# Kernel optimization log

Measured on AMD Instinct MI355X. Metric: run time of the kernel, lower is better.

## Reference

```python
import jax, jax.numpy as jnp
import numpy as np
import math

B, S, H, NH = 8, 2048, 256, 4
DH = H // NH
EPS = 1e-12


def setup_inputs() -> dict:
    key = jax.random.key(0)
    ks = jax.random.split(key, 20)
    g = lambda k, shape: (jax.random.normal(k, shape, jnp.float32) * 0.02)
    inp = {
        "hidden": jax.random.normal(ks[0], (B, S, H), jnp.float32),
        "Wq": g(ks[1], (H, H)), "bq": jnp.zeros((H,), jnp.float32),
        "Wk": g(ks[2], (H, H)), "bk": jnp.zeros((H,), jnp.float32),
        "Wv": g(ks[3], (H, H)), "bv": jnp.zeros((H,), jnp.float32),
        "Wo": g(ks[4], (H, H)), "bo": jnp.zeros((H,), jnp.float32),
        "W1": g(ks[5], (4 * H, H)), "b1": jnp.zeros((4 * H,), jnp.float32),
        "W2": g(ks[6], (H, 4 * H)), "b2": jnp.zeros((H,), jnp.float32),
        "ln1_w": jnp.ones((H,), jnp.float32), "ln1_b": jnp.zeros((H,), jnp.float32),
        "ln2_w": jnp.ones((H,), jnp.float32), "ln2_b": jnp.zeros((H,), jnp.float32),
        "mask": jax.random.randint(ks[7], (B, S), 0, 2, jnp.int32),
    }
    return inp


def _layernorm(x, w, b):
    u = x.mean(-1, keepdims=True)
    s = ((x - u) ** 2).mean(-1, keepdims=True)
    return w * (x - u) / jnp.sqrt(s + EPS) + b


def _gelu_tanh(h):
    return 0.5 * h * (1.0 + jnp.tanh(math.sqrt(2.0 / math.pi) * (h + 0.044715 * h ** 3)))


def _block(hidden, mask, Wq, bq, Wk, bk, Wv, bv, Wo, bo, W1, b1, W2, b2,
           ln1_w, ln1_b, ln2_w, ln2_b):
    # --- attention sublayer (pre-norm + residual) ---
    x = _layernorm(hidden, ln1_w, ln1_b)
    def heads(W, b):  # [B,S,H] -> [B,NH,S,DH]
        return (x @ W.T + b).reshape(B, S, NH, DH).transpose(0, 2, 1, 3)
    q, k, v = heads(Wq, bq), heads(Wk, bk), heads(Wv, bv)
    corr = jnp.einsum("bhqd,bhkd->bhqk", q, k) / math.sqrt(DH)
    # torch code masks QUERY rows: mask [B,S] broadcast over heads and keys
    corr = jnp.where(mask[:, None, :, None] == 0, -1e9, corr)
    prob = jax.nn.softmax(corr, axis=-1)
    attn = jnp.einsum("bhqk,bhkd->bhqd", prob, v)
    attn = attn.transpose(0, 2, 1, 3).reshape(B, S, H) @ Wo.T + bo
    hidden = hidden + attn
    # --- FFN sublayer (pre-norm + residual) ---
    y = _layernorm(hidden, ln2_w, ln2_b)
    h1 = y @ W1.T + b1
    ff = _gelu_tanh(h1) @ W2.T + b2
    return hidden + ff


def reference(hidden, Wq, bq, Wk, bk, Wv, bv, Wo, bo, W1, b1, W2, b2,
              ln1_w, ln1_b, ln2_w, ln2_b, mask):
    return _block(hidden, mask, Wq, bq, Wk, bk, Wv, bv, Wo, bo,
                  W1, b1, W2, b2, ln1_w, ln1_b, ln2_w, ln2_b)
```

## Files before the change

kernel.cpp:

```cpp
#include <hip/hip_runtime.h>
#include <hip/hip_bf16.h>
#include <cstdint>
#include <cstddef>

constexpr int CB  = 8;
constexpr int CS  = 2048;
constexpr int CH  = 256;
constexpr int CNH = 4;
constexpr int CDH = 64;
constexpr int CT  = CB * CS;

typedef __attribute__((ext_vector_type(8)))  __bf16 bf16x8;
typedef __attribute__((ext_vector_type(4)))  float  f32x4;
typedef __attribute__((ext_vector_type(16))) float  f32x16;
typedef __attribute__((ext_vector_type(2)))  int    i32x2;

__device__ __forceinline__ float b2f(unsigned short u) {
    union { float f; unsigned int i; } v; v.i = ((unsigned int)u) << 16; return v.f;
}
__device__ __forceinline__ unsigned short f2b(float f) {
    union { float f; unsigned int i; } v; v.f = f;
    unsigned int r = v.i + 0x7FFFu + ((v.i >> 16) & 1u);
    return (unsigned short)(r >> 16);
}
__device__ __forceinline__ unsigned short f2b_fast(float f) {
    union { float f; unsigned int i; } v; v.f = f;
    return (unsigned short)((v.i + 0x8000u) >> 16);
}
__device__ __forceinline__ unsigned int packbf(float a, float b) {
    return (unsigned int)f2b_fast(a) | ((unsigned int)f2b_fast(b) << 16);
}
__device__ __forceinline__ float fexp2(float x) {
#if __has_builtin(__builtin_amdgcn_exp2f)
    return __builtin_amdgcn_exp2f(x);
#else
    float r; asm("v_exp_f32 %0, %1" : "=v"(r) : "v"(x)); return r;
#endif
}
__device__ __forceinline__ f32x4 mfma16(bf16x8 a, bf16x8 b, f32x4 c) {
    return __builtin_amdgcn_mfma_f32_16x16x32_bf16(a, b, c, 0, 0, 0);
}
__device__ __forceinline__ f32x16 mfma32(bf16x8 a, bf16x8 b, f32x16 c) {
    return __builtin_amdgcn_mfma_f32_32x32x16_bf16(a, b, c, 0, 0, 0);
}
__device__ __forceinline__ f32x16 zero16() {
    f32x16 z;
    #pragma unroll
    for (int i = 0; i < 16; ++i) z[i] = 0.f;
    return z;
}

#define GLOAD_LDS16(gptr, lptr)                                                        \
    __builtin_amdgcn_global_load_lds((const __attribute__((address_space(1))) void*)(gptr), \
                                     (__attribute__((address_space(3))) void*)(lptr), 16, 0, 0)

#define QSCALE 0.1803368801111204f

__global__ __launch_bounds__(256) void detect_kernel(
    const unsigned short* __restrict__ h, int* __restrict__ flag)
{
    __shared__ int s_bad;
    const int tid = threadIdx.x;
    if (tid == 0) s_bad = 0;
    __syncthreads();
    bool bad = false;
    for (int i = tid; i < 2048; i += 256) {
        float v = b2f(h[i]);
        if (!(fabsf(v) < 1e25f)) bad = true;
    }
    if (bad) s_bad = 1;
    __syncthreads();
    if (tid == 0) *flag = s_bad;
}

struct CvtArgs6  { const void* src[6];  void* dst[6];  int n[6]; };
struct CvtArgs11 { const void* src[11]; void* dst[11]; int n[11]; };

__global__ __launch_bounds__(256) void cvt_to_bf16_k(const int* __restrict__ flag, CvtArgs6 a)
{
    const int seg = blockIdx.y, n = a.n[seg];
    const bool inf32 = (*flag != 0);
    const float* sf = (const float*)a.src[seg];
    const unsigned short* sb = (const unsigned short*)a.src[seg];
    unsigned short* d = (unsigned short*)a.dst[seg];
    for (int i = (blockIdx.x * 256 + threadIdx.x) * 4; i < n; i += gridDim.x * 1024) {
        ushort4 o;
        if (inf32) {
            float4 v = *(const float4*)(sf + i);
            o.x = f2b(v.x); o.y = f2b(v.y); o.z = f2b(v.z); o.w = f2b(v.w);
        } else {
            o = *(const ushort4*)(sb + i);
        }
        *(ushort4*)(d + i) = o;
    }
}

__global__ __launch_bounds__(256) void cvt_to_f32_k(const int* __restrict__ flag, CvtArgs11 a)
{
    const int seg = blockIdx.y, n = a.n[seg];
    const bool inf32 = (*flag != 0);
    const float* sf = (const float*)a.src[seg];
    const unsigned short* sb = (const unsigned short*)a.src[seg];
    float* d = (float*)a.dst[seg];
    for (int i = (blockIdx.x * 256 + threadIdx.x) * 4; i < n; i += gridDim.x * 1024) {
        float4 o;
        if (inf32) {
            o = *(const float4*)(sf + i);
        } else {
            ushort4 v = *(const ushort4*)(sb + i);
            o.x = b2f(v.x); o.y = b2f(v.y); o.z = b2f(v.z); o.w = b2f(v.w);
        }
        *(float4*)(d + i) = o;
    }
}

__global__ __launch_bounds__(256) void ln_kernel(
    const float* __restrict__ x, const float* __restrict__ w,
    const float* __restrict__ b, unsigned short* __restrict__ out)
{
    const int wave = threadIdx.x >> 6, lane = threadIdx.x & 63;
    const int token = blockIdx.x * 4 + wave;
    const int c = lane * 4;
    const size_t rowo = (size_t)token * CH + c;
    float4 u = *(const float4*)(x + rowo);
    float v0 = u.x, v1 = u.y, v2 = u.z, v3 = u.w;
    float s = v0 + v1 + v2 + v3;
    float q = v0*v0 + v1*v1 + v2*v2 + v3*v3;
    #pragma unroll
    for (int m = 1; m < 64; m <<= 1) { s += __shfl_xor(s, m, 64); q += __shfl_xor(q, m, 64); }
    float mean = s * (1.0f/256.0f);
    float var  = q * (1.0f/256.0f) - mean*mean;
    float inv  = rsqrtf(var + 1e-12f);
    float4 ww = *(const float4*)(w + c);
    float4 bb = *(const float4*)(b + c);
    ushort4 o;
    o.x = f2b(ww.x * (v0-mean)*inv + bb.x);
    o.y = f2b(ww.y * (v1-mean)*inv + bb.y);
    o.z = f2b(ww.z * (v2-mean)*inv + bb.z);
    o.w = f2b(ww.w * (v3-mean)*inv + bb.w);
    *(ushort4*)(out + rowo) = o;
}

template<bool GELU, bool RESID, bool HEADSTORE, bool OUTF32, bool OUTDYN>
__device__ __forceinline__ void gemm_core(
    const unsigned short* __restrict__ A, const unsigned short* __restrict__ W,
    const float* __restrict__ bias, const float* __restrict__ resid,
    void* __restrict__ out, const int* __restrict__ flag,
    int K, int N, int m0, int n0, float oscale)
{
    __shared__ __align__(16) unsigned short lA[128*32];
    __shared__ __align__(16) unsigned short lB[128*32];
    const int tid  = threadIdx.x;
    const int lane = tid & 63;
    const int wave = tid >> 6;
    const int wr = (wave >> 1) * 64;
    const int wc = (wave & 1) * 64;
    const int g = lane >> 4, r16 = lane & 15;
    const int lrow = lane >> 2;
    const int lch  = lane & 3;

    const f32x4 zero = {0.f, 0.f, 0.f, 0.f};
    f32x4 acc[4][4];
    #pragma unroll
    for (int m = 0; m < 4; ++m)
        #pragma unroll
        for (int n = 0; n < 4; ++n) acc[m][n] = zero;

    for (int k0 = 0; k0 < K; k0 += 32) {
        #pragma unroll
        for (int i = 0; i < 2; ++i) {
            int chunk = wave + i * 4;
            int row = chunk * 16 + lrow;
            const unsigned short* ga = A + (size_t)(m0 + row) * K + k0 + lch * 8;
            GLOAD_LDS16(ga, &lA[chunk * 512]);
            const unsigned short* gw = W + (size_t)(n0 + row) * K + k0 + lch * 8;
            GLOAD_LDS16(gw, &lB[chunk * 512]);
        }
        __syncthreads();
        bf16x8 af[4], wf[4];
        #pragma unroll
        for (int m = 0; m < 4; ++m) af[m] = *(const bf16x8*)&lA[(wr + m*16 + r16) * 32 + g * 8];
        #pragma unroll
        for (int n = 0; n < 4; ++n) wf[n] = *(const bf16x8*)&lB[(wc + n*16 + r16) * 32 + g * 8];
        #pragma unroll
        for (int m = 0; m < 4; ++m)
            #pragma unroll
            for (int n = 0; n < 4; ++n)
                acc[m][n] = mfma16(af[m], wf[n], acc[m][n]);
        __syncthreads();
    }

    const bool of32dyn = OUTDYN ? (*flag != 0) : false;
    #pragma unroll
    for (int n = 0; n < 4; ++n) {
        int col = n0 + wc + n*16 + r16;
        float bv = bias[col];
        #pragma unroll
        for (int m = 0; m < 4; ++m) {
            int row0 = m0 + wr + m*16 + g*4;
            #pragma unroll
            for (int r = 0; r < 4; ++r) {
                int row = row0 + r;
                float v = (acc[m][n][r] + bv) * oscale;
                if (GELU) {
                    float a = 0.79788456080286541f * (v + 0.044715f * v * v * v);
                    v = v * (1.0f / (1.0f + __expf(-2.0f * a)));
                }
                if (RESID) v += resid[(size_t)row * N + col];
                size_t oidx;
                if (HEADSTORE) {
                    int hh = col >> 6, d = col & 63;
                    int bb = row >> 11, ss = row & 2047;
                    oidx = ((((size_t)bb * CNH + hh) * CS) + ss) * CDH + d;
                } else {
                    oidx = (size_t)row * N + col;
                }
                if (OUTF32)      ((float*)out)[oidx] = v;
                else if (OUTDYN) {
                    if (of32dyn) ((float*)out)[oidx] = v;
                    else         ((unsigned short*)out)[oidx] = f2b(v);
                }
                else             ((unsigned short*)out)[oidx] = f2b(v);
            }
        }
    }
}

__global__ __launch_bounds__(256) void k_qkv(
    const unsigned short* __restrict__ xhat,
    const unsigned short* Wq, const float* bq, unsigned short* q,
    const unsigned short* Wk, const float* bk, unsigned short* k,
    const unsigned short* Wv, const float* bv, unsigned short* v)
{
    const unsigned short* W  = blockIdx.z == 0 ? Wq : (blockIdx.z == 1 ? Wk : Wv);
    const float*          bi = blockIdx.z == 0 ? bq : (blockIdx.z == 1 ? bk : bv);
    unsigned short*       o  = blockIdx.z == 0 ? q  : (blockIdx.z == 1 ? k  : v);
    const float osc = blockIdx.z == 0 ? QSCALE : 1.0f;
    gemm_core<false, false, true, false, false>(xhat, W, bi, nullptr, o, nullptr,
                                                CH, CH, blockIdx.x * 128, blockIdx.y * 128, osc);
}

__global__ __launch_bounds__(256) void k_oproj(
    const unsigned short* __restrict__ A, const unsigned short* __restrict__ W,
    const float* __restrict__ bias, const float* __restrict__ resid,
    float* __restrict__ out)
{
    gemm_core<false, true, false, true, false>(A, W, bias, resid, out, nullptr,
                                               CH, CH, blockIdx.x * 128, blockIdx.y * 128, 1.0f);
}

__global__ __launch_bounds__(256) void k_ffn1(
    const unsigned short* __restrict__ A, const unsigned short* __restrict__ W,
    const float* __restrict__ bias, unsigned short* __restrict__ out)
{
    gemm_core<true, false, false, false, false>(A, W, bias, nullptr, out, nullptr,
                                                CH, 4*CH, blockIdx.x * 128, blockIdx.y * 128, 1.0f);
}

__global__ __launch_bounds__(256) void k_ffn2(
    const unsigned short* __restrict__ A, const unsigned short* __restrict__ W,
    const float* __restrict__ bias, const float* __restrict__ resid,
    void* __restrict__ out, const int* __restrict__ flag)
{
    gemm_core<false, true, false, false, true>(A, W, bias, resid, out, flag,
                                               4*CH, CH, blockIdx.x * 128, blockIdx.y * 128, 1.0f);
}

__global__ __launch_bounds__(256) void vtrans_kernel(
    const unsigned short* __restrict__ v, unsigned short* __restrict__ vt)
{
    __shared__ unsigned short T[64 * 72];
    const int bh = blockIdx.y, s0 = blockIdx.x * 64, tid = threadIdx.x;
    const size_t ibase = (size_t)bh * CS * CDH;
    const size_t obase = (size_t)bh * CDH * CS;
    #pragma unroll
    for (int i = 0; i < 2; ++i) {
        int t2 = tid + i * 256;
        int row = t2 >> 3, ch = t2 & 7;
        uint4 dv = *(const uint4*)(v + ibase + (size_t)(s0 + row) * CDH + ch * 8);
        *(uint4*)&T[row * 72 + ch * 8] = dv;
    }
    __syncthreads();
    #pragma unroll
    for (int i = 0; i < 2; ++i) {
        int t2 = tid + i * 256;
        int d = t2 >> 3, ch = t2 & 7;
        unsigned short tmp[8];
        #pragma unroll
        for (int j = 0; j < 8; ++j) tmp[j] = T[(ch * 8 + j) * 72 + d];
        *(uint4*)(vt + obase + (size_t)d * CS + s0 + ch * 8) = *(uint4*)tmp;
    }
}

__global__ __launch_bounds__(512, 4) void attn_kernel(
    const unsigned short* __restrict__ Q, const unsigned short* __restrict__ Kp,
    const unsigned short* __restrict__ Vt, const int* __restrict__ mask,
    unsigned short* __restrict__ out)
{
    __shared__ __align__(16) char lds[65536];

    const int tid = threadIdx.x, lane = tid & 63, wave = tid >> 6;
    const int qb = wave >> 1, kh = wave & 1;
    const int r32 = lane & 31, hi = lane >> 5;
    const int bh = blockIdx.y, bb = bh >> 2, hh = bh & 3;
    const int q0 = blockIdx.x * 128;
    const size_t baseQ = (size_t)bh * CS * CDH;
    const size_t baseT = (size_t)bh * CDH * CS;

    const int qrow = q0 + qb * 32 + r32;
    bf16x8 qf[4];
    {
        const bool live = (mask[bb * CS + qrow] != 0);
        #pragma unroll
        for (int dw = 0; dw < 4; ++dw) {
            uint4 v = {0u, 0u, 0u, 0u};
            if (live) v = *(const uint4*)(Q + baseQ + (size_t)qrow * CDH + dw * 16 + hi * 8);
            qf[dw] = *(bf16x8*)&v;
        }
    }

#define STAGE(BUF, KT) do {                                                             \
        _Pragma("unroll")                                                               \
        for (int i = 0; i < 2; ++i) {                                                   \
            const int slot0 = i * 512 + wave * 64;                                      \
            const int slot  = slot0 + lane;                                             \
            const int kw = slot >> 7, kk2 = slot & 127;                                 \
            GLOAD_LDS16(Kp + baseQ + (size_t)((KT) + kk2) * CDH + kw * 8,               \
                        lds + (BUF) * 16384 + slot0 * 16);                              \
            const int vc = slot >> 6, vd = slot & 63;                                   \
            GLOAD_LDS16(Vt + baseT + (size_t)vd * CS + (KT) + vc * 8,                   \
                        lds + 32768 + (BUF) * 16384 + slot0 * 16);                      \
        } } while (0)

    f32x16 o0 = zero16(), o1 = zero16();
    float psum = 0.f;

    STAGE(0, 0);
    __syncthreads();

    for (int t = 0; t < CS / 128; ++t) {
        const int buf = t & 1;
        const int kt = t * 128;
        if (t + 1 < CS / 128) STAGE(buf ^ 1, kt + 128);

        const char* kbase = lds + buf * 16384;
        const char* vbase = lds + 32768 + buf * 16384;

        f32x16 sT0 = zero16(), sT1 = zero16();
        __builtin_amdgcn_s_setprio(1);
        #pragma unroll
        for (int dw = 0; dw < 4; ++dw) {
            const char* cb = kbase + (dw * 2 + hi) * 2048;
            bf16x8 k0 = *(const bf16x8*)(cb + (kh * 64 + r32) * 16);
            bf16x8 k1 = *(const bf16x8*)(cb + (kh * 64 + 32 + r32) * 16);
            sT0 = mfma32(k0, qf[dw], sT0);
            sT1 = mfma32(k1, qf[dw], sT1);
        }
        __builtin_amdgcn_s_setprio(0);

#define PROCKB(SREG, KB) do {                                                           \
            float p[16];                                                                \
            _Pragma("unroll")                                                           \
            for (int r = 0; r < 16; ++r) { p[r] = fexp2((SREG)[r]); psum += p[r]; }     \
            _Pragma("unroll")                                                           \
            for (int w = 0; w < 2; ++w) {                                               \
                unsigned int a01 = packbf(p[w*8+0], p[w*8+1]);                          \
                unsigned int a23 = packbf(p[w*8+2], p[w*8+3]);                          \
                unsigned int b01 = packbf(p[w*8+4], p[w*8+5]);                          \
                unsigned int b23 = packbf(p[w*8+6], p[w*8+7]);                          \
                unsigned int ap0, ap1, ap2, ap3;                                        \
                {                                                                       \
                    i32x2 s1 = __builtin_amdgcn_permlane32_swap((int)a01, (int)b01, false, false); \
                    i32x2 s2 = __builtin_amdgcn_permlane32_swap((int)a23, (int)b23, false, false); \
                    ap0 = (unsigned int)s1.x; ap2 = (unsigned int)s1.y;                 \
                    ap1 = (unsigned int)s2.x; ap3 = (unsigned int)s2.y;                 \
                }                                                                       \
                union { unsigned int u[4]; bf16x8 v; } apv;                             \
                apv.u[0] = ap0; apv.u[1] = ap1; apv.u[2] = ap2; apv.u[3] = ap3;         \
                const char* vb2 = vbase + ((kh * 4 + (KB) * 2 + w) * 2 + hi) * 1024;    \
                bf16x8 v0 = *(const bf16x8*)(vb2 + r32 * 16);                           \
                bf16x8 v1 = *(const bf16x8*)(vb2 + (32 + r32) * 16);                    \
                o0 = mfma32(apv.v, v0, o0);                                             \
                o1 = mfma32(apv.v, v1, o1);                                             \
            } } while (0)

        PROCKB(sT0, 0);
        PROCKB(sT1, 1);
#undef PROCKB

        __syncthreads();
    }

    float ps = psum + __shfl_xor(psum, 32, 64);
    float* lsum = (float*)(lds + 32768);
    float* Oex  = (float*)lds;
    if (lane < 32) lsum[(qb * 2 + kh) * 32 + r32] = ps;
    if (kh == 1) {
        #pragma unroll
        for (int r = 0; r < 16; ++r) {
            const int qr = (r & 3) + 8 * (r >> 2) + 4 * hi;
            Oex[(qb * 32 + qr) * 64 + r32]      = o0[r];
            Oex[(qb * 32 + qr) * 64 + 32 + r32] = o1[r];
        }
    }
    __syncthreads();
    if (kh == 0) {
        #pragma unroll
        for (int r = 0; r < 16; ++r) {
            const int qr = (r & 3) + 8 * (r >> 2) + 4 * hi;
            const float l = lsum[(qb * 2 + 0) * 32 + qr] + lsum[(qb * 2 + 1) * 32 + qr];
            const float inv = 1.0f / l;
            const float u0 = (o0[r] + Oex[(qb * 32 + qr) * 64 + r32]) * inv;
            const float u1 = (o1[r] + Oex[(qb * 32 + qr) * 64 + 32 + r32]) * inv;
            const size_t ob = (size_t)(bb * CS + q0 + qb * 32 + qr) * CH + hh * CDH;
            out[ob + r32]      = f2b(u0);
            out[ob + 32 + r32] = f2b(u1);
        }
    }
#undef STAGE
}

extern "C" void kernel_launch(void* const* d_in, const int* in_sizes, int n_in,
                              void* d_out, int out_size, void* d_ws, size_t ws_size,
                              hipStream_t stream)
{
    const void* hidden = d_in[0];
    const void* Wq = d_in[1];  const void* bq = d_in[2];
    const void* Wk = d_in[3];  const void* bk = d_in[4];
    const void* Wv = d_in[5];  const void* bv = d_in[6];
    const void* Wo = d_in[7];  const void* bo = d_in[8];
    const void* W1 = d_in[9];  const void* b1 = d_in[10];
    const void* W2 = d_in[11]; const void* b2 = d_in[12];
    const void* ln1w = d_in[13]; const void* ln1b = d_in[14];
    const void* ln2w = d_in[15]; const void* ln2b = d_in[16];
    const int* mask = (const int*)d_in[17];

    char* ws = (char*)d_ws;
    const size_t KB = 1u << 10, MB = 1u << 20;
    int*            flag  = (int*)ws;
    float*          bqf   = (float*)(ws + 4*KB);
    float*          bkf   = (float*)(ws + 8*KB);
    float*          bvf   = (float*)(ws + 12*KB);
    float*          bof   = (float*)(ws + 16*KB);
    float*          b1f   = (float*)(ws + 20*KB);
    float*          b2f_  = (float*)(ws + 28*KB);
    float*          ln1wf = (float*)(ws + 32*KB);
    float*          ln1bf = (float*)(ws + 36*KB);
    float*          ln2wf = (float*)(ws + 40*KB);
    float*          ln2bf = (float*)(ws + 44*KB);
    unsigned short* Wqb   = (unsigned short*)(ws + 1*MB);
    unsigned short* Wkb   = (unsigned short*)(ws + 1*MB + 256*KB);
    unsigned short* Wvb   = (unsigned short*)(ws + 1*MB + 512*KB);
    unsigned short* Wob   = (unsigned short*)(ws + 1*MB + 768*KB);
    unsigned short* W1b   = (unsigned short*)(ws + 2*MB);
    unsigned short* W2b   = (unsigned short*)(ws + 2*MB + 512*KB);
    float*          hf32  = (float*)(ws + 3*MB);
    unsigned short* xhat  = (unsigned short*)(ws + 19*MB);
    unsigned short* qb    = (unsigned short*)(ws + 27*MB);
    unsigned short* kb    = (unsigned short*)(ws + 35*MB);
    unsigned short* vb    = (unsigned short*)(ws + 43*MB);
    unsigned short* attnb = xhat;
    float*          hid2f = (float*)(ws + 35*MB);
    unsigned short* vtb   = (unsigned short*)(ws + 51*MB);
    unsigned short* yhat  = qb;
    unsigned short* h1g   = (unsigned short*)(ws + 51*MB);

    dim3 blk(256);
    detect_kernel<<<1, blk, 0, stream>>>((const unsigned short*)hidden, flag);

    CvtArgs6 cw;
    cw.src[0]=Wq;  cw.dst[0]=Wqb; cw.n[0]=CH*CH;
    cw.src[1]=Wk;  cw.dst[1]=Wkb; cw.n[1]=CH*CH;
    cw.src[2]=Wv;  cw.dst[2]=Wvb; cw.n[2]=CH*CH;
    cw.src[3]=Wo;  cw.dst[3]=Wob; cw.n[3]=CH*CH;
    cw.src[4]=W1;  cw.dst[4]=W1b; cw.n[4]=4*CH*CH;
    cw.src[5]=W2;  cw.dst[5]=W2b; cw.n[5]=4*CH*CH;
    cvt_to_bf16_k<<<dim3(64, 6), blk, 0, stream>>>(flag, cw);

    CvtArgs11 cf;
    cf.src[0]=hidden; cf.dst[0]=hf32;  cf.n[0]=CT*CH;
    cf.src[1]=bq;     cf.dst[1]=bqf;   cf.n[1]=CH;
    cf.src[2]=bk;     cf.dst[2]=bkf;   cf.n[2]=CH;
    cf.src[3]=bv;     cf.dst[3]=bvf;   cf.n[3]=CH;
    cf.src[4]=bo;     cf.dst[4]=bof;   cf.n[4]=CH;
    cf.src[5]=b1;     cf.dst[5]=b1f;   cf.n[5]=4*CH;
    cf.src[6]=b2;     cf.dst[6]=b2f_;  cf.n[6]=CH;
    cf.src[7]=ln1w;   cf.dst[7]=ln1wf; cf.n[7]=CH;
    cf.src[8]=ln1b;   cf.dst[8]=ln1bf; cf.n[8]=CH;
    cf.src[9]=ln2w;   cf.dst[9]=ln2wf; cf.n[9]=CH;
    cf.src[10]=ln2b;  cf.dst[10]=ln2bf;cf.n[10]=CH;
    cvt_to_f32_k<<<dim3(512, 11), blk, 0, stream>>>(flag, cf);

    ln_kernel<<<CT / 4, blk, 0, stream>>>(hf32, ln1wf, ln1bf, xhat);
    k_qkv<<<dim3(CT / 128, CH / 128, 3), blk, 0, stream>>>(xhat, Wqb, bqf, qb,
                                                           Wkb, bkf, kb, Wvb, bvf, vb);
    vtrans_kernel<<<dim3(CS / 64, CB * CNH), blk, 0, stream>>>(vb, vtb);
    attn_kernel<<<dim3(CS / 128, CB * CNH), dim3(512), 0, stream>>>(qb, kb, vtb, mask, attnb);
    k_oproj<<<dim3(CT / 128, CH / 128), blk, 0, stream>>>(attnb, Wob, bof, hf32, hid2f);
    ln_kernel<<<CT / 4, blk, 0, stream>>>(hid2f, ln2wf, ln2bf, yhat);
    k_ffn1<<<dim3(CT / 128, (4 * CH) / 128), blk, 0, stream>>>(yhat, W1b, b1f, h1g);
    k_ffn2<<<dim3(CT / 128, CH / 128), blk, 0, stream>>>(h1g, W2b, b2f_, hid2f,
                                                         d_out, flag);
}
```

Baseline: 167.8 us.

## Store residual stream in bf16 and reorder GEMM grids for weight reuse

```diff
diff --git a/kernel.cpp b/kernel.cpp
--- a/kernel.cpp
+++ b/kernel.cpp
@@ -23,12 +23,10 @@
     unsigned int r = v.i + 0x7FFFu + ((v.i >> 16) & 1u);
     return (unsigned short)(r >> 16);
 }
-__device__ __forceinline__ unsigned short f2b_fast(float f) {
-    union { float f; unsigned int i; } v; v.f = f;
-    return (unsigned short)((v.i + 0x8000u) >> 16);
-}
 __device__ __forceinline__ unsigned int packbf(float a, float b) {
-    return (unsigned int)f2b_fast(a) | ((unsigned int)f2b_fast(b) << 16);
+    float2 t; t.x = a; t.y = b;
+    __hip_bfloat162 h = __float22bfloat162_rn(t);
+    union { __hip_bfloat162 h; unsigned int u; } c; c.h = h; return c.u;
 }
 __device__ __forceinline__ float fexp2(float x) {
 #if __has_builtin(__builtin_amdgcn_exp2f)
@@ -73,10 +71,10 @@
     if (tid == 0) *flag = s_bad;
 }
 
-struct CvtArgs6  { const void* src[6];  void* dst[6];  int n[6]; };
-struct CvtArgs11 { const void* src[11]; void* dst[11]; int n[11]; };
-
-__global__ __launch_bounds__(256) void cvt_to_bf16_k(const int* __restrict__ flag, CvtArgs6 a)
+struct CvtW { const void* src[7]; void* dst[7]; int n[7]; };
+struct CvtB { const void* src[10]; void* dst[10]; int n[10]; };
+
+__global__ __launch_bounds__(256) void cvt_wb_k(const int* __restrict__ flag, CvtW a)
 {
     const int seg = blockIdx.y, n = a.n[seg];
     const bool inf32 = (*flag != 0);
@@ -95,14 +93,15 @@
     }
 }
 
-__global__ __launch_bounds__(256) void cvt_to_f32_k(const int* __restrict__ flag, CvtArgs11 a)
+__global__ __launch_bounds__(256) void cvt_bf_k(const int* __restrict__ flag, CvtB a)
 {
     const int seg = blockIdx.y, n = a.n[seg];
     const bool inf32 = (*flag != 0);
     const float* sf = (const float*)a.src[seg];
     const unsigned short* sb = (const unsigned short*)a.src[seg];
     float* d = (float*)a.dst[seg];
-    for (int i = (blockIdx.x * 256 + threadIdx.x) * 4; i < n; i += gridDim.x * 1024) {
+    const int i = threadIdx.x * 4;
+    if (i < n) {
         float4 o;
         if (inf32) {
             o = *(const float4*)(sf + i);
@@ -115,15 +114,15 @@
 }
 
 __global__ __launch_bounds__(256) void ln_kernel(
-    const float* __restrict__ x, const float* __restrict__ w,
+    const unsigned short* __restrict__ x, const float* __restrict__ w,
     const float* __restrict__ b, unsigned short* __restrict__ out)
 {
     const int wave = threadIdx.x >> 6, lane = threadIdx.x & 63;
     const int token = blockIdx.x * 4 + wave;
     const int c = lane * 4;
     const size_t rowo = (size_t)token * CH + c;
-    float4 u = *(const float4*)(x + rowo);
-    float v0 = u.x, v1 = u.y, v2 = u.z, v3 = u.w;
+    ushort4 u = *(const ushort4*)(x + rowo);
+    float v0 = b2f(u.x), v1 = b2f(u.y), v2 = b2f(u.z), v3 = b2f(u.w);
     float s = v0 + v1 + v2 + v3;
     float q = v0*v0 + v1*v1 + v2*v2 + v3*v3;
     #pragma unroll
@@ -141,10 +140,10 @@
     *(ushort4*)(out + rowo) = o;
 }
 
-template<bool GELU, bool RESID, bool HEADSTORE, bool OUTF32, bool OUTDYN>
+template<bool GELU, bool RESID, bool HEADSTORE, bool OUTDYN>
 __device__ __forceinline__ void gemm_core(
     const unsigned short* __restrict__ A, const unsigned short* __restrict__ W,
-    const float* __restrict__ bias, const float* __restrict__ resid,
+    const float* __restrict__ bias, const unsigned short* __restrict__ resid,
     void* __restrict__ out, const int* __restrict__ flag,
     int K, int N, int m0, int n0, float oscale)
 {
@@ -206,7 +205,7 @@
                     float a = 0.79788456080286541f * (v + 0.044715f * v * v * v);
                     v = v * (1.0f / (1.0f + __expf(-2.0f * a)));
                 }
-                if (RESID) v += resid[(size_t)row * N + col];
+                if (RESID) v += b2f(resid[(size_t)row * N + col]);
                 size_t oidx;
                 if (HEADSTORE) {
                     int hh = col >> 6, d = col & 63;
@@ -215,12 +214,8 @@
                 } else {
                     oidx = (size_t)row * N + col;
                 }
-                if (OUTF32)      ((float*)out)[oidx] = v;
-                else if (OUTDYN) {
-                    if (of32dyn) ((float*)out)[oidx] = v;
-                    else         ((unsigned short*)out)[oidx] = f2b(v);
-                }
-                else             ((unsigned short*)out)[oidx] = f2b(v);
+                if (OUTDYN && of32dyn) ((float*)out)[oidx] = v;
+                else                   ((unsigned short*)out)[oidx] = f2b(v);
             }
         }
     }
@@ -232,38 +227,41 @@
     const unsigned short* Wk, const float* bk, unsigned short* k,
     const unsigned short* Wv, const float* bv, unsigned short* v)
 {
-    const unsigned short* W  = blockIdx.z == 0 ? Wq : (blockIdx.z == 1 ? Wk : Wv);
-    const float*          bi = blockIdx.z == 0 ? bq : (blockIdx.z == 1 ? bk : bv);
-    unsigned short*       o  = blockIdx.z == 0 ? q  : (blockIdx.z == 1 ? k  : v);
-    const float osc = blockIdx.z == 0 ? QSCALE : 1.0f;
-    gemm_core<false, false, true, false, false>(xhat, W, bi, nullptr, o, nullptr,
-                                                CH, CH, blockIdx.x * 128, blockIdx.y * 128, osc);
+    const int z  = blockIdx.x % 3;
+    const int n0 = (blockIdx.x / 3) * 128;
+    const int m0 = blockIdx.y * 128;
+    const unsigned short* W  = z == 0 ? Wq : (z == 1 ? Wk : Wv);
+    const float*          bi = z == 0 ? bq : (z == 1 ? bk : bv);
+    unsigned short*       o  = z == 0 ? q  : (z == 1 ? k  : v);
+    const float osc = z == 0 ? QSCALE : 1.0f;
+    gemm_core<false, false, true, false>(xhat, W, bi, nullptr, o, nullptr,
+                                         CH, CH, m0, n0, osc);
 }
 
 __global__ __launch_bounds__(256) void k_oproj(
     const unsigned short* __restrict__ A, const unsigned short* __restrict__ W,
-    const float* __restrict__ bias, const float* __restrict__ resid,
-    float* __restrict__ out)
-{
-    gemm_core<false, true, false, true, false>(A, W, bias, resid, out, nullptr,
-                                               CH, CH, blockIdx.x * 128, blockIdx.y * 128, 1.0f);
+    const float* __restrict__ bias, const unsigned short* __restrict__ resid,
+    unsigned short* __restrict__ out)
+{
+    gemm_core<false, true, false, false>(A, W, bias, resid, out, nullptr,
+                                         CH, CH, blockIdx.y * 128, blockIdx.x * 128, 1.0f);
 }
 
 __global__ __launch_bounds__(256) void k_ffn1(
     const unsigned short* __restrict__ A, const unsigned short* __restrict__ W,
     const float* __restrict__ bias, unsigned short* __restrict__ out)
 {
-    gemm_core<true, false, false, false, false>(A, W, bias, nullptr, out, nullptr,
-                                                CH, 4*CH, blockIdx.x * 128, blockIdx.y * 128, 1.0f);
+    gemm_core<true, false, false, false>(A, W, bias, nullptr, out, nullptr,
+                                         CH, 4*CH, blockIdx.y * 128, blockIdx.x * 128, 1.0f);
 }
 
 __global__ __launch_bounds__(256) void k_ffn2(
     const unsigned short* __restrict__ A, const unsigned short* __restrict__ W,
-    const float* __restrict__ bias, const float* __restrict__ resid,
+    const float* __restrict__ bias, const unsigned short* __restrict__ resid,
     void* __restrict__ out, const int* __restrict__ flag)
 {
-    gemm_core<false, true, false, false, true>(A, W, bias, resid, out, flag,
-                                               4*CH, CH, blockIdx.x * 128, blockIdx.y * 128, 1.0f);
+    gemm_core<false, true, false, true>(A, W, bias, resid, out, flag,
+                                        4*CH, CH, blockIdx.y * 128, blockIdx.x * 128, 1.0f);
 }
 
 __global__ __launch_bounds__(256) void vtrans_kernel(
@@ -454,51 +452,51 @@
     unsigned short* Wob   = (unsigned short*)(ws + 1*MB + 768*KB);
     unsigned short* W1b   = (unsigned short*)(ws + 2*MB);
     unsigned short* W2b   = (unsigned short*)(ws + 2*MB + 512*KB);
-    float*          hf32  = (float*)(ws + 3*MB);
-    unsigned short* xhat  = (unsigned short*)(ws + 19*MB);
-    unsigned short* qb    = (unsigned short*)(ws + 27*MB);
-    unsigned short* kb    = (unsigned short*)(ws + 35*MB);
-    unsigned short* vb    = (unsigned short*)(ws + 43*MB);
+    unsigned short* hb16  = (unsigned short*)(ws + 3*MB);
+    unsigned short* xhat  = (unsigned short*)(ws + 11*MB);
+    unsigned short* qb    = (unsigned short*)(ws + 19*MB);
+    unsigned short* kb    = (unsigned short*)(ws + 27*MB);
+    unsigned short* vb    = (unsigned short*)(ws + 35*MB);
+    unsigned short* vtb   = (unsigned short*)(ws + 43*MB);
     unsigned short* attnb = xhat;
-    float*          hid2f = (float*)(ws + 35*MB);
-    unsigned short* vtb   = (unsigned short*)(ws + 51*MB);
-    unsigned short* yhat  = qb;
+    unsigned short* hid2b = qb;
+    unsigned short* yhat  = kb;
     unsigned short* h1g   = (unsigned short*)(ws + 51*MB);
 
     dim3 blk(256);
     detect_kernel<<<1, blk, 0, stream>>>((const unsigned short*)hidden, flag);
 
-    CvtArgs6 cw;
-    cw.src[0]=Wq;  cw.dst[0]=Wqb; cw.n[0]=CH*CH;
-    cw.src[1]=Wk;  cw.dst[1]=Wkb; cw.n[1]=CH*CH;
-    cw.src[2]=Wv;  cw.dst[2]=Wvb; cw.n[2]=CH*CH;
-    cw.src[3]=Wo;  cw.dst[3]=Wob; cw.n[3]=CH*CH;
-    cw.src[4]=W1;  cw.dst[4]=W1b; cw.n[4]=4*CH*CH;
-    cw.src[5]=W2;  cw.dst[5]=W2b; cw.n[5]=4*CH*CH;
-    cvt_to_bf16_k<<<dim3(64, 6), blk, 0, stream>>>(flag, cw);
-
-    CvtArgs11 cf;
-    cf.src[0]=hidden; cf.dst[0]=hf32;  cf.n[0]=CT*CH;
-    cf.src[1]=bq;     cf.dst[1]=bqf;   cf.n[1]=CH;
-    cf.src[2]=bk;     cf.dst[2]=bkf;   cf.n[2]=CH;
-    cf.src[3]=bv;     cf.dst[3]=bvf;   cf.n[3]=CH;
-    cf.src[4]=bo;     cf.dst[4]=bof;   cf.n[4]=CH;
-    cf.src[5]=b1;     cf.dst[5]=b1f;   cf.n[5]=4*CH;
-    cf.src[6]=b2;     cf.dst[6]=b2f_;  cf.n[6]=CH;
-    cf.src[7]=ln1w;   cf.dst[7]=ln1wf; cf.n[7]=CH;
-    cf.src[8]=ln1b;   cf.dst[8]=ln1bf; cf.n[8]=CH;
-    cf.src[9]=ln2w;   cf.dst[9]=ln2wf; cf.n[9]=CH;
-    cf.src[10]=ln2b;  cf.dst[10]=ln2bf;cf.n[10]=CH;
-    cvt_to_f32_k<<<dim3(512, 11), blk, 0, stream>>>(flag, cf);
-
-    ln_kernel<<<CT / 4, blk, 0, stream>>>(hf32, ln1wf, ln1bf, xhat);
-    k_qkv<<<dim3(CT / 128, CH / 128, 3), blk, 0, stream>>>(xhat, Wqb, bqf, qb,
-                                                           Wkb, bkf, kb, Wvb, bvf, vb);
+    CvtW cw;
+    cw.src[0]=Wq;  cw.dst[0]=Wqb;  cw.n[0]=CH*CH;
+    cw.src[1]=Wk;  cw.dst[1]=Wkb;  cw.n[1]=CH*CH;
+    cw.src[2]=Wv;  cw.dst[2]=Wvb;  cw.n[2]=CH*CH;
+    cw.src[3]=Wo;  cw.dst[3]=Wob;  cw.n[3]=CH*CH;
+    cw.src[4]=W1;  cw.dst[4]=W1b;  cw.n[4]=4*CH*CH;
+    cw.src[5]=W2;  cw.dst[5]=W2b;  cw.n[5]=4*CH*CH;
+    cw.src[6]=hidden; cw.dst[6]=hb16; cw.n[6]=CT*CH;
+    cvt_wb_k<<<dim3(256, 7), blk, 0, stream>>>(flag, cw);
+
+    CvtB cf;
+    cf.src[0]=bq;    cf.dst[0]=bqf;   cf.n[0]=CH;
+    cf.src[1]=bk;    cf.dst[1]=bkf;   cf.n[1]=CH;
+    cf.src[2]=bv;    cf.dst[2]=bvf;   cf.n[2]=CH;
+    cf.src[3]=bo;    cf.dst[3]=bof;   cf.n[3]=CH;
+    cf.src[4]=b1;    cf.dst[4]=b1f;   cf.n[4]=4*CH;
+    cf.src[5]=b2;    cf.dst[5]=b2f_;  cf.n[5]=CH;
+    cf.src[6]=ln1w;  cf.dst[6]=ln1wf; cf.n[6]=CH;
+    cf.src[7]=ln1b;  cf.dst[7]=ln1bf; cf.n[7]=CH;
+    cf.src[8]=ln2w;  cf.dst[8]=ln2wf; cf.n[8]=CH;
+    cf.src[9]=ln2b;  cf.dst[9]=ln2bf; cf.n[9]=CH;
+    cvt_bf_k<<<dim3(1, 10), blk, 0, stream>>>(flag, cf);
+
+    ln_kernel<<<CT / 4, blk, 0, stream>>>(hb16, ln1wf, ln1bf, xhat);
+    k_qkv<<<dim3(6, CT / 128), blk, 0, stream>>>(xhat, Wqb, bqf, qb,
+                                                 Wkb, bkf, kb, Wvb, bvf, vb);
     vtrans_kernel<<<dim3(CS / 64, CB * CNH), blk, 0, stream>>>(vb, vtb);
     attn_kernel<<<dim3(CS / 128, CB * CNH), dim3(512), 0, stream>>>(qb, kb, vtb, mask, attnb);
-    k_oproj<<<dim3(CT / 128, CH / 128), blk, 0, stream>>>(attnb, Wob, bof, hf32, hid2f);
-    ln_kernel<<<CT / 4, blk, 0, stream>>>(hid2f, ln2wf, ln2bf, yhat);
-    k_ffn1<<<dim3(CT / 128, (4 * CH) / 128), blk, 0, stream>>>(yhat, W1b, b1f, h1g);
-    k_ffn2<<<dim3(CT / 128, CH / 128), blk, 0, stream>>>(h1g, W2b, b2f_, hid2f,
+    k_oproj<<<dim3(CH / 128, CT / 128), blk, 0, stream>>>(attnb, Wob, bof, hb16, hid2b);
+    ln_kernel<<<CT / 4, blk, 0, stream>>>(hid2b, ln2wf, ln2bf, yhat);
+    k_ffn1<<<dim3((4 * CH) / 128, CT / 128), blk, 0, stream>>>(yhat, W1b, b1f, h1g);
+    k_ffn2<<<dim3(CH / 128, CT / 128), blk, 0, stream>>>(h1g, W2b, b2f_, hid2b,
                                                          d_out, flag);
 }
```

Measured after the change: 172.1 us. +2.5%, slower.
